# Optimization experiments

Measured on AMD Instinct MI355X. Metric: run time of the kernel, lower is better.

The kernel has to match this reference:

```python
import jax, jax.numpy as jnp
import numpy as np

N_SIGMA = 3
FG_W = 1.0
W_INST, W_VAR, W_SEED = 1.0, 10.0, 1.0
N_IDS = 16  # instance ids 1..16; id 0 = background
B, C, D, H, W = 4, 7, 32, 192, 192


def setup_inputs() -> dict:
    key = jax.random.key(0)
    k1, k2, k3, k4 = jax.random.split(key, 4)
    prediction = jax.random.normal(k1, (B, C, D, H, W), dtype=jnp.float32)
    instances = jax.random.randint(k2, (B, D, H, W), 0, N_IDS + 1, dtype=jnp.int32)
    labels = jax.random.randint(k3, (B, D, H, W), 0, 2, dtype=jnp.int32)
    center_images = jax.random.randint(k4, (B, D, H, W), 0, 2) > 0
    # coordinate buffer, pixel_{x,y,z}=1, grid dims == volume dims
    xm = jnp.broadcast_to(jnp.linspace(0.0, 1.0, W).reshape(1, 1, W), (D, H, W))
    ym = jnp.broadcast_to(jnp.linspace(0.0, 1.0, H).reshape(1, H, 1), (D, H, W))
    zm = jnp.broadcast_to(jnp.linspace(0.0, 1.0, D).reshape(D, 1, 1), (D, H, W))
    xyzm = jnp.stack([xm, ym, zm], 0).astype(jnp.float32)  # [3,D,H,W]
    return {"prediction": prediction, "instances": instances, "labels": labels,
            "center_images": center_images, "xyzm": xyzm}


def _lovasz_hinge(logits, gt):
    # logits, gt: flat [N]; gt in {0,1} float. Lovasz grad is detached (Variable(grad) in torch impl).
    signs = 2.0 * gt - 1.0
    errors = 1.0 - logits * signs
    order = jnp.argsort(-errors)  # descending
    errors_sorted = errors[order]
    gt_sorted = gt[order]
    gts = gt_sorted.sum()
    intersection = gts - jnp.cumsum(gt_sorted)
    union = gts + jnp.cumsum(1.0 - gt_sorted)
    jaccard = 1.0 - intersection / union
    grad = jnp.concatenate([jaccard[:1], jaccard[1:] - jaccard[:-1]])
    return jnp.dot(jax.nn.relu(errors_sorted), jax.lax.stop_gradient(grad))


def reference(prediction, instances, labels, center_images, xyzm):
    bsz = prediction.shape[0]
    dhw = prediction.shape[2] * prediction.shape[3] * prediction.shape[4]
    spatial_emb = jnp.tanh(prediction[:, :3]) + xyzm[None]             # [B,3,D,H,W]
    sigma = prediction[:, 3:3 + N_SIGMA]                               # [B,3,D,H,W]
    seed_map = jax.nn.sigmoid(prediction[:, 3 + N_SIGMA])              # [B,D,H,W]

    bg_seed = jnp.sum(jnp.where(labels == 0, seed_map ** 2, 0.0), axis=(1, 2, 3))  # [B]

    ids = jnp.arange(1, N_IDS + 1)

    def per_instance(se_b, sigma_b, seed_b, inst_b, iid):
        m = (inst_b == iid).astype(jnp.float32)                         # [D,H,W]
        cnt = m.sum()
        exists = cnt > 0
        safe = jnp.maximum(cnt, 1.0)
        center = jnp.sum(xyzm * m[None], axis=(1, 2, 3)) / safe         # [3]
        s_mean = jnp.sum(sigma_b * m[None], axis=(1, 2, 3)) / safe      # [n_sigma]
        var = jnp.sum(((sigma_b - jax.lax.stop_gradient(s_mean)[:, None, None, None]) ** 2) * m[None]) / (N_SIGMA * safe)
        s_exp = jnp.exp(s_mean * 10.0)[:, None, None, None]
        dist = jnp.exp(-jnp.sum(((se_b - center[:, None, None, None]) ** 2) * s_exp, axis=0))  # [D,H,W]
        inst_l = _lovasz_hinge((dist * 2.0 - 1.0).reshape(-1), m.reshape(-1))
        seed_l = FG_W * jnp.sum(((seed_b - jax.lax.stop_gradient(dist)) ** 2) * m)
        z = jnp.float32(0.0)
        return (jnp.where(exists, var, z), jnp.where(exists, inst_l, z),
                jnp.where(exists, seed_l, z), exists.astype(jnp.float32))

    def per_batch(se_b, sigma_b, seed_b, inst_b):
        v, il, sl, ex = jax.vmap(per_instance, in_axes=(None, None, None, None, 0))(
            se_b, sigma_b, seed_b, inst_b, ids)
        obj = ex.sum()
        denom = jnp.maximum(obj, 1.0)
        return v.sum() / denom, il.sum() / denom, sl.sum()

    var_b, inst_lb, seed_lb = jax.vmap(per_batch)(spatial_emb, sigma, seed_map, instances)
    seed_total = (seed_lb + bg_seed) / dhw
    loss_inst = inst_lb.sum() * W_INST / bsz
    loss_var = var_b.sum() * W_VAR / bsz
    loss_seed = seed_total.sum() * W_SEED / bsz
    loss_sum = loss_inst + loss_var + loss_seed + prediction.sum() * 0.0
    return jnp.stack([loss_inst, loss_var, loss_seed, loss_sum])
```

## Files before the change

### kernel.cpp

```cpp
#include <hip/hip_runtime.h>

#define NID  16
#define BB   4
#define HH   192
#define WW   192
#define DHW  1179648
#define KB   256

#define P1_ROWS   24
#define P1_ITERS  72

#define P3_CHUNKS 192
#define P3_CHUNK  6144
#define SUBT      6
#define SUBN      1024
#define SUBIT     4

#define WS_STATS 0
#define WS_BG8   512
#define WS_SEED8 544
#define WS_INSTL 576
#define WS_HIST  640
#define WS_TOTAL (640 + 64*2*KB)

__device__ __forceinline__ float ftanh(float x) {
    float t = __expf(2.f * x);
    return 1.f - 2.f / (t + 1.f);
}
__device__ __forceinline__ float fsigmoid(float x) {
    return 1.f / (1.f + __expf(-x));
}
__device__ __forceinline__ float wred(float v) {
    for (int off = 32; off > 0; off >>= 1) v += __shfl_down(v, off, 64);
    return v;
}
__device__ __forceinline__ void xyz_of(int v, float& x, float& y, float& z) {
    int w = v % WW;
    int t = v / WW;
    int h = t % HH;
    int d = t / HH;
    x = (float)w * (1.f / 191.f);
    y = (float)h * (1.f / 191.f);
    z = (float)d * (1.f / 31.f);
}

#define REP8(M) M(0) M(1) M(2) M(3) M(4) M(5) M(6) M(7)

__global__ __launch_bounds__(256) void pass1_stats(
    const float* __restrict__ pred, const int* __restrict__ inst,
    const int* __restrict__ labels, float* __restrict__ ws)
{
    __shared__ float part[128];
    const int b    = blockIdx.y;
    const int tid  = threadIdx.x;
    const int wv   = tid >> 6;
    const int lane = tid & 63;
    const int idb0 = (wv & 1) * 8;

    const float* p3 = pred + (size_t)(b * 7 + 3) * DHW;
    const int*   ib = inst   + (size_t)b * DHW;
    const int*   lb = labels + (size_t)b * DHW;
    const int row0 = blockIdx.x * P1_ROWS;

    if (wv < 2) {
        unsigned G00=0u,G01=0u,G02=0u,G03=0u,G04=0u,G05=0u,G06=0u,G07=0u;
        unsigned G10=0u,G11=0u,G12=0u,G13=0u,G14=0u,G15=0u,G16=0u,G17=0u;
        float bgacc = 0.f;
        for (int it = 0; it < P1_ITERS; ++it) {
            const int seg = it % 3, r = it / 3;
            const int row = row0 + r;
            const int w   = seg * 64 + lane;
            const int v   = row * WW + w;
            const int id  = ib[v];
            if (wv == 0) {
                const float seed = fsigmoid(p3[3 * DHW + v]);
                if (lb[v] == 0) bgacc += seed * seed;
            }
            const unsigned p0 = (unsigned)w | (1u << 17);
            const unsigned p1 = (unsigned)(row % HH) | ((unsigned)(row / HH) << 17);
            const int idx = id - 1 - idb0;
            #define GEO(Q) { const bool e = (idx == Q); \
                             G0##Q += e ? p0 : 0u; G1##Q += e ? p1 : 0u; }
            REP8(GEO)
            #undef GEO
        }
        #define GRED(Q) { \
            float c  = wred((float)(G0##Q >> 17)); \
            float sx = wred((float)(G0##Q & 0x1FFFFu) * (1.f / 191.f)); \
            float sy = wred((float)(G1##Q & 0x1FFFFu) * (1.f / 191.f)); \
            float sz = wred((float)(G1##Q >> 17)      * (1.f / 31.f)); \
            if (lane == 0) { float* pp = &part[(idb0 + Q) * 8]; \
                             pp[0] = c; pp[1] = sx; pp[2] = sy; pp[3] = sz; } }
        REP8(GRED)
        #undef GRED
        if (wv == 0) {
            const float r = wred(bgacc);
            if (lane == 0) atomicAdd(&ws[WS_BG8 + b * 8 + (blockIdx.x & 7)], r);
        }
    } else {
        float SA0=0.f,SA1=0.f,SA2=0.f,SA3=0.f,SA4=0.f,SA5=0.f,SA6=0.f,SA7=0.f;
        float SB0=0.f,SB1=0.f,SB2=0.f,SB3=0.f,SB4=0.f,SB5=0.f,SB6=0.f,SB7=0.f;
        float SC0=0.f,SC1=0.f,SC2=0.f,SC3=0.f,SC4=0.f,SC5=0.f,SC6=0.f,SC7=0.f;
        float SD0=0.f,SD1=0.f,SD2=0.f,SD3=0.f,SD4=0.f,SD5=0.f,SD6=0.f,SD7=0.f;
        for (int it = 0; it < P1_ITERS; ++it) {
            const int seg = it % 3, r = it / 3;
            const int v   = (row0 + r) * WW + seg * 64 + lane;
            const int id  = ib[v];
            const float s0 = p3[v], s1 = p3[DHW + v], s2 = p3[2 * DHW + v];
            const float sq = s0 * s0 + s1 * s1 + s2 * s2;
            const int idx = id - 1 - idb0;
            #define SIG(Q) { const float m = (idx == Q) ? 1.f : 0.f; \
                SA##Q = fmaf(m, s0, SA##Q); SB##Q = fmaf(m, s1, SB##Q); \
                SC##Q = fmaf(m, s2, SC##Q); SD##Q = fmaf(m, sq, SD##Q); }
            REP8(SIG)
            #undef SIG
        }
        #define SRED(Q) { \
            float r0 = wred(SA##Q), r1 = wred(SB##Q); \
            float r2 = wred(SC##Q), r3 = wred(SD##Q); \
            if (lane == 0) { float* pp = &part[(idb0 + Q) * 8 + 4]; \
                             pp[0] = r0; pp[1] = r1; pp[2] = r2; pp[3] = r3; } }
        REP8(SRED)
        #undef SRED
    }
    __syncthreads();
    if (tid < 128) {
        const float pv = part[tid];
        if (pv != 0.f) atomicAdd(&ws[WS_STATS + b * 128 + tid], pv);
    }
}

__global__ __launch_bounds__(256) void pass3_hist(
    const float* __restrict__ pred, const int* __restrict__ inst,
    float* __restrict__ ws)
{
    __shared__ float4 sev[SUBN];
    __shared__ unsigned cntFB[2][NID][KB + 1];
    __shared__ float ctrs[NID][8];
    __shared__ float sred[4];

    const int b   = blockIdx.y;
    const int tid = threadIdx.x;
    const int rep = (tid >> 5) & 1;
    const int rot = tid & 15;

    for (int i = tid; i < 2 * NID * (KB + 1); i += 256) ((unsigned*)cntFB)[i] = 0u;
    if (tid < NID) {
        const float* s = ws + WS_STATS + (size_t)(b * NID + tid) * 8;
        const float cnt = s[0];
        const float safe = fmaxf(cnt, 1.f);
        const float m0 = s[4] / safe, m1 = s[5] / safe, m2 = s[6] / safe;
        ctrs[tid][0] = s[1] / safe;
        ctrs[tid][1] = s[2] / safe;
        ctrs[tid][2] = s[3] / safe;
        ctrs[tid][3] = __expf(10.f * m0);
        ctrs[tid][4] = __expf(10.f * m1);
        ctrs[tid][5] = __expf(10.f * m2);
        ctrs[tid][6] = 0.f;
        ctrs[tid][7] = (cnt > 0.f) ? 1.f : 0.f;
    }
    __syncthreads();

    const float* pb = pred + (size_t)b * 7 * DHW;
    const int*   ib = inst + (size_t)b * DHW;

    float sacc = 0.f;
    const int base0 = blockIdx.x * P3_CHUNK;

    for (int sub = 0; sub < SUBT; ++sub) {
        const int vb = base0 + sub * SUBN;
        for (int it = 0; it < SUBIT; ++it) {
            const int i = it * 256 + tid;
            const int v = vb + i;
            float x, y, z; xyz_of(v, x, y, z);
            const float se0 = ftanh(pb[v])           + x;
            const float se1 = ftanh(pb[DHW + v])     + y;
            const float se2 = ftanh(pb[2 * DHW + v]) + z;
            const float seed = fsigmoid(pb[6 * DHW + v]);
            const unsigned id = (unsigned)ib[v];
            const unsigned sw = (__float_as_uint(seed) & ~0xFFu) | id;
            sev[i] = make_float4(se0, se1, se2, __uint_as_float(sw));
        }
        __syncthreads();
        for (int p = 0; p < 4; ++p) {
            float cx[4], cy[4], cz[4], e0[4], e1[4], e2[4];
            int iidq[4];
            #pragma unroll
            for (int j = 0; j < 4; ++j) {
                const int iid = (p * 4 + j + rot) & 15;
                iidq[j] = iid;
                cx[j] = ctrs[iid][0]; cy[j] = ctrs[iid][1]; cz[j] = ctrs[iid][2];
                e0[j] = ctrs[iid][3]; e1[j] = ctrs[iid][4]; e2[j] = ctrs[iid][5];
            }
            for (int it = 0; it < SUBIT; ++it) {
                const int i = it * 256 + tid;
                const float4 sv = sev[i];
                const unsigned sw = __float_as_uint(sv.w);
                const int id = (int)(sw & 0xFFu);
                const float seed = sv.w;
                #pragma unroll
                for (int j = 0; j < 4; ++j) {
                    const float d0 = sv.x - cx[j];
                    const float d1 = sv.y - cy[j];
                    const float d2 = sv.z - cz[j];
                    const float q2 = d0 * d0 * e0[j] + d1 * d1 * e1[j] + d2 * d2 * e2[j];
                    const float dist = __expf(-q2);
                    const bool m = (id == iidq[j] + 1);
                    const float e = m ? (2.f - 2.f * dist) : (2.f * dist);
                    int k = (int)(e * 128.f);
                    k = min(max(k, 0), KB - 1);
                    const unsigned val = m ? 1u : (k ? 0x10000u : 0u);
                    if (m) { const float ds = seed - dist; sacc += ds * ds; }
                    if (val) atomicAdd(&cntFB[rep][iidq[j]][k], val);
                }
            }
        }
        __syncthreads();
    }

    float* gh = ws + WS_HIST;
    for (int i = tid; i < NID * KB; i += 256) {
        const int iid = i >> 8, k = i & (KB - 1);
        const unsigned c = cntFB[0][iid][k] + cntFB[1][iid][k];
        float* basep = gh + (size_t)(b * NID + iid) * 2 * KB;
        const float cf = (float)(c & 0xFFFFu);
        const float cb = (float)(c >> 16);
        if (cf != 0.f) atomicAdd(&basep[k], cf);
        if (cb != 0.f) atomicAdd(&basep[KB + k], cb);
    }
    float v = sacc;
    for (int off = 32; off > 0; off >>= 1) v += __shfl_down(v, off, 64);
    if ((tid & 63) == 0) sred[tid >> 6] = v;
    __syncthreads();
    if (tid == 0)
        atomicAdd(&ws[WS_SEED8 + b * 8 + (blockIdx.x & 7)],
                  sred[0] + sred[1] + sred[2] + sred[3]);
}

__global__ __launch_bounds__(256) void pass4_lovasz(float* __restrict__ ws)
{
    const int t = blockIdx.x;
    const int j = threadIdx.x;
    __shared__ float sF[KB], sB[KB];
    __shared__ double red[KB];

    const float P = ws[WS_STATS + t * 8];
    const float* gh = ws + WS_HIST + (size_t)t * 2 * KB;

    const int k = KB - 1 - j;
    const float nF = gh[k], nB = gh[KB + k];
    const float mid = ((float)k + 0.5f) * (1.f / 128.f);
    const float rF = nF * mid, rB = nB * mid;

    sF[j] = nF; sB[j] = nB;
    __syncthreads();
    for (int off = 1; off < KB; off <<= 1) {
        float a = 0.f, c = 0.f;
        if (j >= off) { a = sF[j - off]; c = sB[j - off]; }
        __syncthreads();
        sF[j] += a; sB[j] += c;
        __syncthreads();
    }
    double contrib = 0.0;
    if (P > 0.f) {
        const double Bb = (double)sB[j] - (double)nB;
        const double U0 = (double)P + Bb;
        const double Fafter = (double)sF[j];
        contrib = (double)rF / U0
                + (double)rB * ((double)P - Fafter) / (U0 * (U0 + (double)nB));
    }
    red[j] = contrib;
    __syncthreads();
    for (int off = KB / 2; off > 0; off >>= 1) {
        if (j < off) red[j] += red[j + off];
        __syncthreads();
    }
    if (j == 0) ws[WS_INSTL + t] = (float)red[0];
}

__global__ void pass5_final(const float* __restrict__ ws, float* __restrict__ out)
{
    const int t = threadIdx.x;
    __shared__ float pl[3][4];
    if (t < 4) {
        float obj = 0.f, v = 0.f, i2 = 0.f;
        for (int i = 0; i < NID; ++i) {
            const int u = t * NID + i;
            const float* s = ws + WS_STATS + (size_t)u * 8;
            const float cnt = s[0];
            i2 += ws[WS_INSTL + u];
            if (cnt > 0.f) {
                obj += 1.f;
                const float m0 = s[4] / cnt, m1 = s[5] / cnt, m2 = s[6] / cnt;
                v += (s[7] - cnt * (m0 * m0 + m1 * m1 + m2 * m2)) / (3.f * cnt);
            }
        }
        float sb = 0.f, bg = 0.f;
        for (int j = 0; j < 8; ++j) {
            sb += ws[WS_SEED8 + t * 8 + j];
            bg += ws[WS_BG8   + t * 8 + j];
        }
        const float denom = fmaxf(obj, 1.f);
        pl[0][t] = i2 / denom;
        pl[1][t] = v / denom;
        pl[2][t] = (sb + bg) / (float)DHW;
    }
    __syncthreads();
    if (t == 0) {
        const float linst = (pl[0][0] + pl[0][1] + pl[0][2] + pl[0][3]) * (1.0f / BB);
        const float lvar  = (pl[1][0] + pl[1][1] + pl[1][2] + pl[1][3]) * (10.0f / BB);
        const float lseed = (pl[2][0] + pl[2][1] + pl[2][2] + pl[2][3]) * (1.0f / BB);
        out[0] = linst;
        out[1] = lvar;
        out[2] = lseed;
        out[3] = linst + lvar + lseed;
    }
}

extern "C" void kernel_launch(void* const* d_in, const int* in_sizes, int n_in,
                              void* d_out, int out_size, void* d_ws, size_t ws_size,
                              hipStream_t stream)
{
    const float* pred   = (const float*)d_in[0];
    const int*   inst   = (const int*)  d_in[1];
    const int*   labels = (const int*)  d_in[2];
    float* ws  = (float*)d_ws;
    float* out = (float*)d_out;

    hipMemsetAsync(d_ws, 0, (size_t)WS_TOTAL * sizeof(float), stream);

    dim3 grid1(256, BB);
    dim3 grid3(P3_CHUNKS, BB);
    pass1_stats<<<grid1, 256, 0, stream>>>(pred, inst, labels, ws);
    pass3_hist <<<grid3, 256, 0, stream>>>(pred, inst, ws);
    pass4_lovasz<<<64, KB, 0, stream>>>(ws);
    pass5_final<<<1, 64, 0, stream>>>(ws, out);
}
```

Baseline: 337.4 us.

## Rebalance stats pass, widen histogram instance batch, replicate global hist, fuse final

The stats pass stops splitting waves by task (geometry vs sigma). Each wave pair now covers half the rows and accumulates all statistics, so the load is balanced across waves and the id/pred loads are shared. The histogram pass processes 8 instances per sweep instead of 4 with precomputed row pointers, and writes into 8 replicated global histogram copies to cut global atomic contention. The Lovasz pass sums the copies and uses a last-block counter to fuse the final reduction, removing one launch. This costs more registers and a larger workspace memset.

```diff
diff --git a/kernel.cpp b/kernel.cpp
--- a/kernel.cpp
+++ b/kernel.cpp
@@ -6,9 +6,10 @@
 #define WW   192
 #define DHW  1179648
 #define KB   256
+#define NCOPY 8
 
 #define P1_ROWS   24
-#define P1_ITERS  72
+#define P1_ITERS  36
 
 #define P3_CHUNKS 192
 #define P3_CHUNK  6144
@@ -20,8 +21,9 @@
 #define WS_BG8   512
 #define WS_SEED8 544
 #define WS_INSTL 576
-#define WS_HIST  640
-#define WS_TOTAL (640 + 64*2*KB)
+#define WS_CTR   640
+#define WS_HIST  648
+#define WS_TOTAL (648 + NCOPY*64*2*KB)
 
 __device__ __forceinline__ float ftanh(float x) {
     float t = __expf(2.f * x);
@@ -50,82 +52,72 @@
     const float* __restrict__ pred, const int* __restrict__ inst,
     const int* __restrict__ labels, float* __restrict__ ws)
 {
-    __shared__ float part[128];
-    const int b    = blockIdx.y;
-    const int tid  = threadIdx.x;
-    const int wv   = tid >> 6;
-    const int lane = tid & 63;
-    const int idb0 = (wv & 1) * 8;
+    __shared__ float part[2][128];
+    const int b     = blockIdx.y;
+    const int tid   = threadIdx.x;
+    const int wv    = tid >> 6;
+    const int lane  = tid & 63;
+    const int wpair = wv >> 1;
+    const int half  = wv & 1;
+    const int idb0  = half * 8;
 
     const float* p3 = pred + (size_t)(b * 7 + 3) * DHW;
     const int*   ib = inst   + (size_t)b * DHW;
     const int*   lb = labels + (size_t)b * DHW;
-    const int row0 = blockIdx.x * P1_ROWS;
-
-    if (wv < 2) {
-        unsigned G00=0u,G01=0u,G02=0u,G03=0u,G04=0u,G05=0u,G06=0u,G07=0u;
-        unsigned G10=0u,G11=0u,G12=0u,G13=0u,G14=0u,G15=0u,G16=0u,G17=0u;
-        float bgacc = 0.f;
-        for (int it = 0; it < P1_ITERS; ++it) {
-            const int seg = it % 3, r = it / 3;
-            const int row = row0 + r;
-            const int w   = seg * 64 + lane;
-            const int v   = row * WW + w;
-            const int id  = ib[v];
-            if (wv == 0) {
-                const float seed = fsigmoid(p3[3 * DHW + v]);
-                if (lb[v] == 0) bgacc += seed * seed;
-            }
-            const unsigned p0 = (unsigned)w | (1u << 17);
-            const unsigned p1 = (unsigned)(row % HH) | ((unsigned)(row / HH) << 17);
-            const int idx = id - 1 - idb0;
-            #define GEO(Q) { const bool e = (idx == Q); \
-                             G0##Q += e ? p0 : 0u; G1##Q += e ? p1 : 0u; }
-            REP8(GEO)
-            #undef GEO
-        }
-        #define GRED(Q) { \
-            float c  = wred((float)(G0##Q >> 17)); \
-            float sx = wred((float)(G0##Q & 0x1FFFFu) * (1.f / 191.f)); \
-            float sy = wred((float)(G1##Q & 0x1FFFFu) * (1.f / 191.f)); \
-            float sz = wred((float)(G1##Q >> 17)      * (1.f / 31.f)); \
-            if (lane == 0) { float* pp = &part[(idb0 + Q) * 8]; \
-                             pp[0] = c; pp[1] = sx; pp[2] = sy; pp[3] = sz; } }
-        REP8(GRED)
-        #undef GRED
-        if (wv == 0) {
-            const float r = wred(bgacc);
-            if (lane == 0) atomicAdd(&ws[WS_BG8 + b * 8 + (blockIdx.x & 7)], r);
-        }
-    } else {
-        float SA0=0.f,SA1=0.f,SA2=0.f,SA3=0.f,SA4=0.f,SA5=0.f,SA6=0.f,SA7=0.f;
-        float SB0=0.f,SB1=0.f,SB2=0.f,SB3=0.f,SB4=0.f,SB5=0.f,SB6=0.f,SB7=0.f;
-        float SC0=0.f,SC1=0.f,SC2=0.f,SC3=0.f,SC4=0.f,SC5=0.f,SC6=0.f,SC7=0.f;
-        float SD0=0.f,SD1=0.f,SD2=0.f,SD3=0.f,SD4=0.f,SD5=0.f,SD6=0.f,SD7=0.f;
-        for (int it = 0; it < P1_ITERS; ++it) {
-            const int seg = it % 3, r = it / 3;
-            const int v   = (row0 + r) * WW + seg * 64 + lane;
-            const int id  = ib[v];
-            const float s0 = p3[v], s1 = p3[DHW + v], s2 = p3[2 * DHW + v];
-            const float sq = s0 * s0 + s1 * s1 + s2 * s2;
-            const int idx = id - 1 - idb0;
-            #define SIG(Q) { const float m = (idx == Q) ? 1.f : 0.f; \
-                SA##Q = fmaf(m, s0, SA##Q); SB##Q = fmaf(m, s1, SB##Q); \
-                SC##Q = fmaf(m, s2, SC##Q); SD##Q = fmaf(m, sq, SD##Q); }
-            REP8(SIG)
-            #undef SIG
-        }
-        #define SRED(Q) { \
-            float r0 = wred(SA##Q), r1 = wred(SB##Q); \
-            float r2 = wred(SC##Q), r3 = wred(SD##Q); \
-            if (lane == 0) { float* pp = &part[(idb0 + Q) * 8 + 4]; \
-                             pp[0] = r0; pp[1] = r1; pp[2] = r2; pp[3] = r3; } }
-        REP8(SRED)
-        #undef SRED
+    const int row0 = blockIdx.x * P1_ROWS + wpair * 12;
+
+    unsigned G00=0u,G01=0u,G02=0u,G03=0u,G04=0u,G05=0u,G06=0u,G07=0u;
+    unsigned G10=0u,G11=0u,G12=0u,G13=0u,G14=0u,G15=0u,G16=0u,G17=0u;
+    float SA0=0.f,SA1=0.f,SA2=0.f,SA3=0.f,SA4=0.f,SA5=0.f,SA6=0.f,SA7=0.f;
+    float SB0=0.f,SB1=0.f,SB2=0.f,SB3=0.f,SB4=0.f,SB5=0.f,SB6=0.f,SB7=0.f;
+    float SC0=0.f,SC1=0.f,SC2=0.f,SC3=0.f,SC4=0.f,SC5=0.f,SC6=0.f,SC7=0.f;
+    float SD0=0.f,SD1=0.f,SD2=0.f,SD3=0.f,SD4=0.f,SD5=0.f,SD6=0.f,SD7=0.f;
+    float bgacc = 0.f;
+
+    for (int it = 0; it < P1_ITERS; ++it) {
+        const int seg = it % 3, r = it / 3;
+        const int row = row0 + r;
+        const int w   = seg * 64 + lane;
+        const int v   = row * WW + w;
+        const int id  = ib[v];
+        const float s0 = p3[v], s1 = p3[DHW + v], s2 = p3[2 * DHW + v];
+        const float sq = s0 * s0 + s1 * s1 + s2 * s2;
+        if (half == 0) {
+            const float seed = fsigmoid(p3[3 * DHW + v]);
+            if (lb[v] == 0) bgacc += seed * seed;
+        }
+        const unsigned p0 = (unsigned)w | (1u << 17);
+        const unsigned p1 = (unsigned)(row % HH) | ((unsigned)(row / HH) << 17);
+        const int idx = id - 1 - idb0;
+        #define ACC(Q) { const bool e = (idx == Q); \
+            G0##Q += e ? p0 : 0u; G1##Q += e ? p1 : 0u; \
+            const float m = e ? 1.f : 0.f; \
+            SA##Q = fmaf(m, s0, SA##Q); SB##Q = fmaf(m, s1, SB##Q); \
+            SC##Q = fmaf(m, s2, SC##Q); SD##Q = fmaf(m, sq, SD##Q); }
+        REP8(ACC)
+        #undef ACC
+    }
+
+    #define GRED(Q) { \
+        float c  = wred((float)(G0##Q >> 17)); \
+        float sx = wred((float)(G0##Q & 0x1FFFFu) * (1.f / 191.f)); \
+        float sy = wred((float)(G1##Q & 0x1FFFFu) * (1.f / 191.f)); \
+        float sz = wred((float)(G1##Q >> 17)      * (1.f / 31.f)); \
+        float r0 = wred(SA##Q), r1 = wred(SB##Q); \
+        float r2 = wred(SC##Q), r3 = wred(SD##Q); \
+        if (lane == 0) { float* pp = &part[wpair][(idb0 + Q) * 8]; \
+            pp[0]=c; pp[1]=sx; pp[2]=sy; pp[3]=sz; \
+            pp[4]=r0; pp[5]=r1; pp[6]=r2; pp[7]=r3; } }
+    REP8(GRED)
+    #undef GRED
+
+    if (half == 0) {
+        const float r = wred(bgacc);
+        if (lane == 0) atomicAdd(&ws[WS_BG8 + b * 8 + (blockIdx.x & 7)], r);
     }
     __syncthreads();
     if (tid < 128) {
-        const float pv = part[tid];
+        const float pv = part[0][tid] + part[1][tid];
         if (pv != 0.f) atomicAdd(&ws[WS_STATS + b * 128 + tid], pv);
     }
 }
@@ -182,13 +174,15 @@
             sev[i] = make_float4(se0, se1, se2, __uint_as_float(sw));
         }
         __syncthreads();
-        for (int p = 0; p < 4; ++p) {
-            float cx[4], cy[4], cz[4], e0[4], e1[4], e2[4];
-            int iidq[4];
+        for (int p = 0; p < 2; ++p) {
+            float cx[8], cy[8], cz[8], e0[8], e1[8], e2[8];
+            int ip1[8];
+            unsigned* rowp[8];
             #pragma unroll
-            for (int j = 0; j < 4; ++j) {
-                const int iid = (p * 4 + j + rot) & 15;
-                iidq[j] = iid;
+            for (int j = 0; j < 8; ++j) {
+                const int iid = (p * 8 + j + rot) & 15;
+                ip1[j]  = iid + 1;
+                rowp[j] = &cntFB[rep][iid][0];
                 cx[j] = ctrs[iid][0]; cy[j] = ctrs[iid][1]; cz[j] = ctrs[iid][2];
                 e0[j] = ctrs[iid][3]; e1[j] = ctrs[iid][4]; e2[j] = ctrs[iid][5];
             }
@@ -199,26 +193,27 @@
                 const int id = (int)(sw & 0xFFu);
                 const float seed = sv.w;
                 #pragma unroll
-                for (int j = 0; j < 4; ++j) {
+                for (int j = 0; j < 8; ++j) {
                     const float d0 = sv.x - cx[j];
                     const float d1 = sv.y - cy[j];
                     const float d2 = sv.z - cz[j];
                     const float q2 = d0 * d0 * e0[j] + d1 * d1 * e1[j] + d2 * d2 * e2[j];
                     const float dist = __expf(-q2);
-                    const bool m = (id == iidq[j] + 1);
-                    const float e = m ? (2.f - 2.f * dist) : (2.f * dist);
-                    int k = (int)(e * 128.f);
+                    const bool m = (id == ip1[j]);
+                    const float t256 = dist * 256.f;
+                    const float kf = m ? (256.f - t256) : t256;
+                    int k = (int)kf;
                     k = min(max(k, 0), KB - 1);
                     const unsigned val = m ? 1u : (k ? 0x10000u : 0u);
                     if (m) { const float ds = seed - dist; sacc += ds * ds; }
-                    if (val) atomicAdd(&cntFB[rep][iidq[j]][k], val);
+                    if (val) atomicAdd(rowp[j] + k, val);
                 }
             }
         }
         __syncthreads();
     }
 
-    float* gh = ws + WS_HIST;
+    float* gh = ws + WS_HIST + (size_t)((blockIdx.x & (NCOPY - 1)) * 64) * 2 * KB;
     for (int i = tid; i < NID * KB; i += 256) {
         const int iid = i >> 8, k = i & (KB - 1);
         const unsigned c = cntFB[0][iid][k] + cntFB[1][iid][k];
@@ -237,18 +232,26 @@
                   sred[0] + sred[1] + sred[2] + sred[3]);
 }
 
-__global__ __launch_bounds__(256) void pass4_lovasz(float* __restrict__ ws)
+__global__ __launch_bounds__(256) void pass4_lovasz(float* __restrict__ ws,
+                                                    float* __restrict__ out)
 {
     const int t = blockIdx.x;
     const int j = threadIdx.x;
     __shared__ float sF[KB], sB[KB];
     __shared__ double red[KB];
+    __shared__ int lastBlk;
+    __shared__ float pl[3][4];
 
     const float P = ws[WS_STATS + t * 8];
-    const float* gh = ws + WS_HIST + (size_t)t * 2 * KB;
+    const float* ghb = ws + WS_HIST + (size_t)t * 2 * KB;
 
     const int k = KB - 1 - j;
-    const float nF = gh[k], nB = gh[KB + k];
+    float nF = 0.f, nB = 0.f;
+    #pragma unroll
+    for (int c = 0; c < NCOPY; ++c) {
+        nF += ghb[(size_t)c * 64 * 2 * KB + k];
+        nB += ghb[(size_t)c * 64 * 2 * KB + KB + k];
+    }
     const float mid = ((float)k + 0.5f) * (1.f / 128.f);
     const float rF = nF * mid, rB = nB * mid;
 
@@ -275,17 +278,20 @@
         if (j < off) red[j] += red[j + off];
         __syncthreads();
     }
-    if (j == 0) ws[WS_INSTL + t] = (float)red[0];
-}
-
-__global__ void pass5_final(const float* __restrict__ ws, float* __restrict__ out)
-{
-    const int t = threadIdx.x;
-    __shared__ float pl[3][4];
-    if (t < 4) {
+    if (j == 0) {
+        ws[WS_INSTL + t] = (float)red[0];
+        __threadfence();
+        const unsigned old = atomicAdd((unsigned*)&ws[WS_CTR], 1u);
+        lastBlk = (old == 63u) ? 1 : 0;
+    }
+    __syncthreads();
+    if (!lastBlk) return;
+    __threadfence();
+
+    if (j < 4) {
         float obj = 0.f, v = 0.f, i2 = 0.f;
         for (int i = 0; i < NID; ++i) {
-            const int u = t * NID + i;
+            const int u = j * NID + i;
             const float* s = ws + WS_STATS + (size_t)u * 8;
             const float cnt = s[0];
             i2 += ws[WS_INSTL + u];
@@ -296,17 +302,17 @@
             }
         }
         float sb = 0.f, bg = 0.f;
-        for (int j = 0; j < 8; ++j) {
-            sb += ws[WS_SEED8 + t * 8 + j];
-            bg += ws[WS_BG8   + t * 8 + j];
+        for (int q = 0; q < 8; ++q) {
+            sb += ws[WS_SEED8 + j * 8 + q];
+            bg += ws[WS_BG8   + j * 8 + q];
         }
         const float denom = fmaxf(obj, 1.f);
-        pl[0][t] = i2 / denom;
-        pl[1][t] = v / denom;
-        pl[2][t] = (sb + bg) / (float)DHW;
-    }
-    __syncthreads();
-    if (t == 0) {
+        pl[0][j] = i2 / denom;
+        pl[1][j] = v / denom;
+        pl[2][j] = (sb + bg) / (float)DHW;
+    }
+    __syncthreads();
+    if (j == 0) {
         const float linst = (pl[0][0] + pl[0][1] + pl[0][2] + pl[0][3]) * (1.0f / BB);
         const float lvar  = (pl[1][0] + pl[1][1] + pl[1][2] + pl[1][3]) * (10.0f / BB);
         const float lseed = (pl[2][0] + pl[2][1] + pl[2][2] + pl[2][3]) * (1.0f / BB);
@@ -333,6 +339,5 @@
     dim3 grid3(P3_CHUNKS, BB);
     pass1_stats<<<grid1, 256, 0, stream>>>(pred, inst, labels, ws);
     pass3_hist <<<grid3, 256, 0, stream>>>(pred, inst, ws);
-    pass4_lovasz<<<64, KB, 0, stream>>>(ws);
-    pass5_final<<<1, 64, 0, stream>>>(ws, out);
-}
+    pass4_lovasz<<<64, KB, 0, stream>>>(ws, out);
+}
```

Measured after the change: 366.0 us. 1.08x slower.
